# Kernel optimization log

Measured on AMD Instinct MI355X. Metric: run time of the kernel, lower is better.

Reference implementation:

```python
import jax, jax.numpy as jnp
import numpy as np

D_MODEL = 1024
D_INNER = 2048
D_STATE = 16
DT_RANK = 64  # ceil(1024/16)
N_LAYERS = 4
SEQ = 4096


def setup_inputs() -> dict:
    key = jax.random.key(0)
    ks = list(jax.random.split(key, 8))
    L, d, di, n, r = N_LAYERS, D_MODEL, D_INNER, D_STATE, DT_RANK
    def rn(k, shape, scale):
        return jax.random.normal(k, shape, dtype=jnp.float32) * scale
    A_init = jnp.tile(jnp.log(jnp.arange(1, n + 1, dtype=jnp.float32))[None, None, :], (L, di, 1))
    return {
        'x': jax.random.normal(ks[0], (SEQ, d), dtype=jnp.float32),
        'pos_enc': jax.random.normal(ks[1], (SEQ, d), dtype=jnp.float32),
        'ln_g': jnp.ones((d,), jnp.float32),
        'ln_b': jnp.zeros((d,), jnp.float32),
        'innorm_g': jnp.ones((L, d), jnp.float32),
        'innorm_b': jnp.zeros((L, d), jnp.float32),
        'in_proj_w': rn(ks[2], (L, 2 * di, d), 0.02),
        'in_proj_b': jnp.zeros((L, 2 * di), jnp.float32),
        'conv_w': rn(ks[3], (L, di, 1, 3), 0.1),
        'conv_b': jnp.zeros((L, di), jnp.float32),
        'deltaBC_w': rn(ks[4], (L, r + 2 * n, di), 0.02),
        'dt_proj_w': rn(ks[5], (L, di, r), 0.02),
        'dt_proj_b': jnp.zeros((L, di), jnp.float32),
        'A_log': A_init,
        'Dp': jnp.ones((L, di), jnp.float32),
        'outnorm_g': jnp.ones((L, di), jnp.float32),
        'outnorm_b': jnp.zeros((L, di), jnp.float32),
        'out_proj_w': rn(ks[6], (L, d, di), 0.02),
        'out_proj_b': jnp.zeros((L, d), jnp.float32),
    }


def _ln(x, g, b, eps):
    mu = jnp.mean(x, axis=-1, keepdims=True)
    var = jnp.mean((x - mu) ** 2, axis=-1, keepdims=True)
    return (x - mu) * jax.lax.rsqrt(var + eps) * g + b


def _selective_scan(u, delta, A, B, C, D):
    # u, delta: [b,l,d]; A: [d,n]; B, C: [b,l,n]; D: [d]
    b, l, d = u.shape
    n = A.shape[1]
    def step(h, inputs):
        d_t, B_t, u_t, C_t = inputs          # [b,d],[b,n],[b,d],[b,n]
        dA = jnp.exp(d_t[:, :, None] * A)    # [b,d,n]
        dBu = (d_t * u_t)[:, :, None] * B_t[:, None, :]
        h = dA * h + dBu
        y = jnp.einsum('bdn,bn->bd', h, C_t)
        return h, y
    h0 = jnp.zeros((b, d, n), u.dtype)
    xs = (jnp.swapaxes(delta, 0, 1), jnp.swapaxes(B, 0, 1),
          jnp.swapaxes(u, 0, 1), jnp.swapaxes(C, 0, 1))
    _, ys = jax.lax.scan(step, h0, xs)       # ys: [l,b,d]
    return jnp.swapaxes(ys, 0, 1) + u * D


def _block(x, innorm_g, innorm_b, in_proj_w, in_proj_b, conv_w, conv_b,
           deltaBC_w, dt_proj_w, dt_proj_b, A_log, Dp, outnorm_g, outnorm_b,
           out_proj_w, out_proj_b):
    skip = x
    h = _ln(x, innorm_g, innorm_b, 1e-5)
    xz = h @ in_proj_w.T + in_proj_b
    x1, z1 = jnp.split(xz, 2, axis=-1)       # [b,s,di] each
    # depthwise conv1d, k=3, pad=1
    xc = jnp.swapaxes(x1, 1, 2)              # [b,di,s]
    xc = jax.lax.conv_general_dilated(xc, conv_w, (1,), [(1, 1)],
                                      feature_group_count=xc.shape[1],
                                      dimension_numbers=('NCH', 'OIH', 'NCH'))
    xc = xc + conv_b[None, :, None]
    u = jnp.swapaxes(xc, 1, 2)               # [b,s,di]
    # SSM
    A = -jnp.exp(A_log)
    dbc = u @ deltaBC_w.T                    # [b,s,r+2n]
    delta, B, C = jnp.split(dbc, [DT_RANK, DT_RANK + D_STATE], axis=-1)
    delta = jax.nn.softplus(delta @ dt_proj_w.T + dt_proj_b)
    y = _selective_scan(u, delta, A, B, C, Dp)
    y = _ln(y, outnorm_g, outnorm_b, 1e-5)
    out = y * jax.nn.silu(z1)
    return out @ out_proj_w.T + out_proj_b + skip


def _forward(x, pos_enc, ln_g, ln_b, innorm_g, innorm_b, in_proj_w, in_proj_b,
             conv_w, conv_b, deltaBC_w, dt_proj_w, dt_proj_b, A_log, Dp,
             outnorm_g, outnorm_b, out_proj_w, out_proj_b):
    enc = _ln(x + pos_enc, ln_g, ln_b, 1e-6)[None]  # [1,s,d]
    for i in range(N_LAYERS):
        enc = _block(enc, innorm_g[i], innorm_b[i], in_proj_w[i], in_proj_b[i],
                     conv_w[i], conv_b[i], deltaBC_w[i], dt_proj_w[i],
                     dt_proj_b[i], A_log[i], Dp[i], outnorm_g[i], outnorm_b[i],
                     out_proj_w[i], out_proj_b[i])
    return enc[0]


def reference(x, pos_enc, ln_g, ln_b, innorm_g, innorm_b, in_proj_w, in_proj_b,
              conv_w, conv_b, deltaBC_w, dt_proj_w, dt_proj_b, A_log, Dp,
              outnorm_g, outnorm_b, out_proj_w, out_proj_b):
    return _forward(x, pos_enc, ln_g, ln_b, innorm_g, innorm_b, in_proj_w,
                    in_proj_b, conv_w, conv_b, deltaBC_w, dt_proj_w, dt_proj_b,
                    A_log, Dp, outnorm_g, outnorm_b, out_proj_w, out_proj_b)
```

## Files before the change

kernel.cpp:

```cpp
#include <hip/hip_runtime.h>
#include <hip/hip_bf16.h>
#include <stdint.h>


#define SEQ     4096
#define DMODEL  1024
#define DINNER  2048
#define NSTATE  16
#define DTRANK  64
#define NLAYERS 4
#define LC      64
#define NC      64

typedef __attribute__((ext_vector_type(8))) short short8v;
typedef __attribute__((ext_vector_type(4))) float f32x4;
typedef __hip_bfloat16 bf16;

__device__ __forceinline__ float b2f(unsigned short x) {
    unsigned int u = ((unsigned int)x) << 16;
    return __builtin_bit_cast(float, u);
}

__device__ __forceinline__ void gld16(const void* gsrc, void* ldst) {
    __builtin_amdgcn_global_load_lds(
        (const __attribute__((address_space(1))) void*)gsrc,
        (__attribute__((address_space(3))) void*)ldst, 16, 0, 0);
}

__device__ __forceinline__ float block_sum(float v, float* red, int nwaves) {
    #pragma unroll
    for (int o = 32; o > 0; o >>= 1) v += __shfl_down(v, o, 64);
    int lane = threadIdx.x & 63, w = threadIdx.x >> 6;
    __syncthreads();
    if (lane == 0) red[w] = v;
    __syncthreads();
    float s = red[0];
    for (int i = 1; i < nwaves; i++) s += red[i];
    return s;
}

template<int WIDTH, typename OutT>
__global__ void ln_kernel(const float* __restrict__ X, const float* __restrict__ X2,
                          const float* __restrict__ g, const float* __restrict__ bta,
                          OutT* __restrict__ out, float eps) {
    constexpr int E = WIDTH / 256;
    __shared__ float red[4];
    int s = blockIdx.x, tid = threadIdx.x;
    size_t base = (size_t)s * WIDTH;
    float v[E]; float sum = 0.f;
    #pragma unroll
    for (int i = 0; i < E; i++) {
        int c = tid + i * 256;
        float t = X[base + c];
        if (X2) t += X2[base + c];
        v[i] = t; sum += t;
    }
    float mu = block_sum(sum, red, 4) * (1.f / WIDTH);
    float sq = 0.f;
    #pragma unroll
    for (int i = 0; i < E; i++) { float d = v[i] - mu; sq += d * d; }
    float var = block_sum(sq, red, 4) * (1.f / WIDTH);
    float rstd = rsqrtf(var + eps);
    #pragma unroll
    for (int i = 0; i < E; i++) {
        int c = tid + i * 256;
        float r = (v[i] - mu) * rstd * g[c] + bta[c];
        out[base + c] = (OutT)r;
    }
}

__global__ void outnorm_silu_kernel(const float* __restrict__ y, const bf16* __restrict__ xz,
                                    const float* __restrict__ g, const float* __restrict__ bta,
                                    bf16* __restrict__ p_bf, float eps) {
    constexpr int WIDTH = DINNER, E = WIDTH / 256;
    __shared__ float red[4];
    int s = blockIdx.x, tid = threadIdx.x;
    size_t base = (size_t)s * WIDTH;
    const unsigned short* xzu = (const unsigned short*)xz;
    float v[E]; float sum = 0.f;
    #pragma unroll
    for (int i = 0; i < E; i++) { int c = tid + i * 256; v[i] = y[base + c]; sum += v[i]; }
    float mu = block_sum(sum, red, 4) * (1.f / WIDTH);
    float sq = 0.f;
    #pragma unroll
    for (int i = 0; i < E; i++) { float d = v[i] - mu; sq += d * d; }
    float var = block_sum(sq, red, 4) * (1.f / WIDTH);
    float rstd = rsqrtf(var + eps);
    #pragma unroll
    for (int i = 0; i < E; i++) {
        int c = tid + i * 256;
        float ln = (v[i] - mu) * rstd * g[c] + bta[c];
        float z = b2f(xzu[(size_t)s * (2 * DINNER) + DINNER + c]);
        float sig = 1.f / (1.f + __expf(-z));
        p_bf[base + c] = __float2bfloat16(ln * (z * sig));
    }
}

__global__ void conv_kernel(const bf16* __restrict__ xz, const float* __restrict__ cw,
                            const float* __restrict__ cb, bf16* __restrict__ u_bf) {
    int t = blockIdx.x * 256 + threadIdx.x;
    int s = t >> 9, c = (t & 511) * 4;
    size_t row = (size_t)s * (2 * DINNER);
    const unsigned short* xp = (const unsigned short*)xz;
    ushort4 z4 = {0, 0, 0, 0};
    ushort4 v0 = *(const ushort4*)(xp + row + c);
    ushort4 vm = (s > 0)       ? *(const ushort4*)(xp + row - 2 * DINNER + c) : z4;
    ushort4 vp = (s < SEQ - 1) ? *(const ushort4*)(xp + row + 2 * DINNER + c) : z4;
    unsigned short o[4];
    float x0[4] = {b2f(v0.x), b2f(v0.y), b2f(v0.z), b2f(v0.w)};
    float xm[4] = {b2f(vm.x), b2f(vm.y), b2f(vm.z), b2f(vm.w)};
    float xp4[4] = {b2f(vp.x), b2f(vp.y), b2f(vp.z), b2f(vp.w)};
    #pragma unroll
    for (int i = 0; i < 4; i++) {
        int ch = c + i;
        float u = cw[ch * 3 + 0] * xm[i] + cw[ch * 3 + 1] * x0[i]
                + cw[ch * 3 + 2] * xp4[i] + cb[ch];
        o[i] = __builtin_bit_cast(unsigned short, __float2bfloat16(u));
    }
    *(ushort4*)((unsigned short*)u_bf + (size_t)s * DINNER + c) = {o[0], o[1], o[2], o[3]};
}

#define CN0 (2 * DINNER * DMODEL)
#define CN1 (DMODEL * DINNER)
#define CN2 (96 * DINNER)
#define CN3 (DINNER * DTRANK)
__global__ void cvt_all_kernel(const float* __restrict__ w0, const float* __restrict__ w1,
                               const float* __restrict__ w2, const float* __restrict__ w3,
                               bf16* __restrict__ o0, bf16* __restrict__ o1,
                               bf16* __restrict__ o2, bf16* __restrict__ o3) {
    size_t i = (size_t)(blockIdx.x * 256 + threadIdx.x) * 4;
    const float* src; bf16* dst;
    if (i < CN0)                   { src = w0; dst = o0; }
    else if (i < CN0 + CN1)        { src = w1; dst = o1; i -= CN0; }
    else if (i < CN0 + CN1 + CN2)  { src = w2; dst = o2; i -= CN0 + CN1; }
    else                           { src = w3; dst = o3; i -= CN0 + CN1 + CN2; }
    float4 v = *(const float4*)(src + i);
    __hip_bfloat162 t0, t1;
    t0.x = __float2bfloat16(v.x); t0.y = __float2bfloat16(v.y);
    t1.x = __float2bfloat16(v.z); t1.y = __float2bfloat16(v.w);
    __hip_bfloat162* o = (__hip_bfloat162*)(dst + i);
    o[0] = t0; o[1] = t1;
}

template<int MODE>
__global__ __launch_bounds__(256, 2)
void mfma_gemm(const bf16* __restrict__ A, int lda,
               const bf16* __restrict__ W, int ldw,
               const float* __restrict__ bias,
               float* __restrict__ C, int ldc,
               const float* __restrict__ res,
               bf16* __restrict__ Cbf,
               int M, int N, int K) {
    __shared__ __attribute__((aligned(16))) short sA[128][32];
    __shared__ __attribute__((aligned(16))) short sB[128][32];
    int tid = threadIdx.x;
    int lane = tid & 63, w = tid >> 6;
    int wm = w >> 1, wn = w & 1;
    int m0 = blockIdx.x * 128, n0 = blockIdx.y * 128;
    int r16 = lane & 15, quad = lane >> 4;
    int ldrow = (lane >> 2);
    int c8 = (lane & 3) * 8;

    if (MODE == 1) {
        int kz = blockIdx.z;
        A += (size_t)kz * K;
        W += (size_t)kz * K;
        C += (size_t)kz * M * 96;
    }

    f32x4 acc[4][4] = {};

    for (int k0 = 0; k0 < K; k0 += 32) {
        __syncthreads();
        #pragma unroll
        for (int j = 0; j < 2; j++) {
            int row = j * 64 + w * 16 + ldrow;
            gld16(A + (size_t)(m0 + row) * lda + k0 + c8,
                  (char*)&sA[0][0] + j * 4096 + w * 1024);
            int nr = n0 + row; if (nr > N - 1) nr = N - 1;
            gld16(W + (size_t)nr * ldw + k0 + c8,
                  (char*)&sB[0][0] + j * 4096 + w * 1024);
        }
        __syncthreads();
        short8v aF[4], bF[4];
        #pragma unroll
        for (int mi = 0; mi < 4; mi++)
            aF[mi] = *(const short8v*)&sA[wm * 64 + mi * 16 + r16][quad * 8];
        #pragma unroll
        for (int ni = 0; ni < 4; ni++)
            bF[ni] = *(const short8v*)&sB[wn * 64 + ni * 16 + r16][quad * 8];
        #pragma unroll
        for (int mi = 0; mi < 4; mi++)
            #pragma unroll
            for (int ni = 0; ni < 4; ni++)
                acc[mi][ni] = __builtin_amdgcn_mfma_f32_16x16x32_bf16(
                    aF[mi], bF[ni], acc[mi][ni], 0, 0, 0);
    }

    #pragma unroll
    for (int mi = 0; mi < 4; mi++) {
        #pragma unroll
        for (int ni = 0; ni < 4; ni++) {
            f32x4 a = acc[mi][ni];
            int col = n0 + wn * 64 + ni * 16 + r16;
            int rbase = m0 + wm * 64 + mi * 16 + quad * 4;
            #pragma unroll
            for (int r = 0; r < 4; r++) {
                int row = rbase + r;
                float v = a[r];
                if (MODE == 0 || MODE == 2 || MODE == 3) v += bias[col];
                if (MODE == 2) v = (v > 20.f) ? v : log1pf(__expf(v));
                if (MODE == 3) v += res[(size_t)row * ldc + col];
                if (MODE == 1) {
                    if (col < 96) C[(size_t)row * 96 + col] = v;
                } else if (MODE == 0) {
                    Cbf[(size_t)row * ldc + col] = __float2bfloat16(v);
                } else {
                    C[(size_t)row * ldc + col] = v;
                }
            }
        }
    }
}

__global__ void reduce_dbc_kernel(const float* __restrict__ p, float* __restrict__ dbc,
                                  bf16* __restrict__ dbc_bf) {
    int i = blockIdx.x * 256 + threadIdx.x;
    const int SP = SEQ * 96;
    float v = p[i] + p[i + SP] + p[i + 2 * SP] + p[i + 3 * SP];
    dbc[i] = v;
    int row = i / 96, c = i - row * 96;
    if (c < DTRANK) dbc_bf[(size_t)row * DTRANK + c] = __float2bfloat16(v);
}

__device__ __forceinline__ bool a_is_neg_integers(const float* a) {
    bool fast = true;
    #pragma unroll
    for (int n = 0; n < NSTATE; n++)
        fast = fast && (__builtin_fabsf(a[n] + (float)(n + 1)) < 1e-3f * (n + 1));
    return fast;
}

__global__ void scan1_kernel(const float* __restrict__ delta, const bf16* __restrict__ u,
                             const float* __restrict__ dbc, const float* __restrict__ A_log,
                             float* __restrict__ h_end, float* __restrict__ dsum) {
    __shared__ __attribute__((aligned(16))) float sB[LC][NSTATE];
    int k = blockIdx.x, d = blockIdx.y * 256 + threadIdx.x;
    int s0 = k * LC, tid = threadIdx.x;
    #pragma unroll
    for (int i = 0; i < 4; i++) {
        int idx = tid + i * 256;
        int r = idx >> 4, n = idx & 15;
        sB[r][n] = dbc[(size_t)(s0 + r) * 96 + DTRANK + n];
    }
    float a[NSTATE];
    #pragma unroll
    for (int n = 0; n < NSTATE; n++) a[n] = -__expf(A_log[(size_t)d * NSTATE + n]);
    bool fast = a_is_neg_integers(a);
    __syncthreads();
    const unsigned short* uu16 = (const unsigned short*)u;
    float h[NSTATE] = {}; float ds = 0.f;
    if (fast) {
        #pragma unroll 2
        for (int r = 0; r < LC; r++) {
            float dl = delta[(size_t)(s0 + r) * DINNER + d];
            float du = dl * b2f(uu16[(size_t)(s0 + r) * DINNER + d]);
            ds += dl;
            float g = __expf(-dl);
            float Bv[NSTATE];
            #pragma unroll
            for (int q = 0; q < 4; q++) *(float4*)&Bv[q * 4] = *(const float4*)&sB[r][q * 4];
            float fac = 1.f;
            #pragma unroll
            for (int n = 0; n < NSTATE; n++) {
                fac *= g;
                h[n] = fac * h[n] + du * Bv[n];
            }
        }
    } else {
        #pragma unroll 2
        for (int r = 0; r < LC; r++) {
            float dl = delta[(size_t)(s0 + r) * DINNER + d];
            float du = dl * b2f(uu16[(size_t)(s0 + r) * DINNER + d]);
            ds += dl;
            float Bv[NSTATE];
            #pragma unroll
            for (int q = 0; q < 4; q++) *(float4*)&Bv[q * 4] = *(const float4*)&sB[r][q * 4];
            #pragma unroll
            for (int n = 0; n < NSTATE; n++)
                h[n] = __expf(dl * a[n]) * h[n] + du * Bv[n];
        }
    }
    #pragma unroll
    for (int n = 0; n < NSTATE; n++)
        h_end[((size_t)k * NSTATE + n) * DINNER + d] = h[n];
    dsum[(size_t)k * DINNER + d] = ds;
}

__global__ void scan2_kernel(const float* __restrict__ A_log, const float* __restrict__ dsum,
                             const float* __restrict__ h_end, float* __restrict__ hinit) {
    int id = blockIdx.x * 256 + threadIdx.x;
    int d = id & (DINNER - 1), n = id >> 11;
    float a = -__expf(A_log[(size_t)d * NSTATE + n]);
    float h = 0.f;
    for (int k = 0; k < NC; k++) {
        size_t off = ((size_t)k * NSTATE + n) * DINNER + d;
        hinit[off] = h;
        h = __expf(a * dsum[(size_t)k * DINNER + d]) * h + h_end[off];
    }
}

__global__ void scan3_kernel(float* __restrict__ delta_y, const bf16* __restrict__ u,
                             const float* __restrict__ dbc, const float* __restrict__ A_log,
                             const float* __restrict__ Dp, const float* __restrict__ hinit) {
    __shared__ __attribute__((aligned(16))) float sB[LC][NSTATE];
    __shared__ __attribute__((aligned(16))) float sC[LC][NSTATE];
    int k = blockIdx.x, d = blockIdx.y * 256 + threadIdx.x;
    int s0 = k * LC, tid = threadIdx.x;
    #pragma unroll
    for (int i = 0; i < 8; i++) {
        int idx = tid + i * 256;
        int r = idx >> 5, c = idx & 31;
        float v = dbc[(size_t)(s0 + r) * 96 + DTRANK + c];
        if (c < 16) sB[r][c] = v; else sC[r][c - 16] = v;
    }
    float a[NSTATE];
    #pragma unroll
    for (int n = 0; n < NSTATE; n++) a[n] = -__expf(A_log[(size_t)d * NSTATE + n]);
    bool fast = a_is_neg_integers(a);
    float h[NSTATE];
    #pragma unroll
    for (int n = 0; n < NSTATE; n++)
        h[n] = hinit[((size_t)k * NSTATE + n) * DINNER + d];
    float dpv = Dp[d];
    __syncthreads();
    const unsigned short* uu16 = (const unsigned short*)u;
    if (fast) {
        #pragma unroll 2
        for (int r = 0; r < LC; r++) {
            float dl = delta_y[(size_t)(s0 + r) * DINNER + d];
            float uu = b2f(uu16[(size_t)(s0 + r) * DINNER + d]);
            float du = dl * uu;
            float g = __expf(-dl);
            float Bv[NSTATE], Cv[NSTATE];
            #pragma unroll
            for (int q = 0; q < 4; q++) {
                *(float4*)&Bv[q * 4] = *(const float4*)&sB[r][q * 4];
                *(float4*)&Cv[q * 4] = *(const float4*)&sC[r][q * 4];
            }
            float y = uu * dpv;
            float fac = 1.f;
            #pragma unroll
            for (int n = 0; n < NSTATE; n++) {
                fac *= g;
                h[n] = fac * h[n] + du * Bv[n];
                y += h[n] * Cv[n];
            }
            delta_y[(size_t)(s0 + r) * DINNER + d] = y;
        }
    } else {
        #pragma unroll 2
        for (int r = 0; r < LC; r++) {
            float dl = delta_y[(size_t)(s0 + r) * DINNER + d];
            float uu = b2f(uu16[(size_t)(s0 + r) * DINNER + d]);
            float du = dl * uu;
            float Bv[NSTATE], Cv[NSTATE];
            #pragma unroll
            for (int q = 0; q < 4; q++) {
                *(float4*)&Bv[q * 4] = *(const float4*)&sB[r][q * 4];
                *(float4*)&Cv[q * 4] = *(const float4*)&sC[r][q * 4];
            }
            float y = uu * dpv;
            #pragma unroll
            for (int n = 0; n < NSTATE; n++) {
                h[n] = __expf(dl * a[n]) * h[n] + du * Bv[n];
                y += h[n] * Cv[n];
            }
            delta_y[(size_t)(s0 + r) * DINNER + d] = y;
        }
    }
}

extern "C" void kernel_launch(void* const* d_in, const int* in_sizes, int n_in,
                              void* d_out, int out_size, void* d_ws, size_t ws_size,
                              hipStream_t stream) {
    const float* x         = (const float*)d_in[0];
    const float* pos       = (const float*)d_in[1];
    const float* ln_g      = (const float*)d_in[2];
    const float* ln_b      = (const float*)d_in[3];
    const float* innorm_g  = (const float*)d_in[4];
    const float* innorm_b  = (const float*)d_in[5];
    const float* in_proj_w = (const float*)d_in[6];
    const float* in_proj_b = (const float*)d_in[7];
    const float* conv_w    = (const float*)d_in[8];
    const float* conv_b    = (const float*)d_in[9];
    const float* deltaBC_w = (const float*)d_in[10];
    const float* dt_proj_w = (const float*)d_in[11];
    const float* dt_proj_b = (const float*)d_in[12];
    const float* A_log     = (const float*)d_in[13];
    const float* Dp        = (const float*)d_in[14];
    const float* outnorm_g = (const float*)d_in[15];
    const float* outnorm_b = (const float*)d_in[16];
    const float* out_proj_w= (const float*)d_in[17];
    const float* out_proj_b= (const float*)d_in[18];

    float* enc = (float*)d_out;
    char* ws = (char*)d_ws;
    const size_t MB = 1024 * 1024;
    bf16*  h_bf   = (bf16*) (ws + 0);
    bf16*  p_bf   = (bf16*) (ws + 0);
    bf16*  xz_bf  = (bf16*) (ws + 16 * MB);
    float* dlt    = (float*)(ws + 48 * MB);
    float* dbcp   = (float*)(ws + 48 * MB);
    bf16*  u_bf   = (bf16*) (ws + 80 * MB);
    float* dbc    = (float*)(ws + 96 * MB);
    bf16*  dbc_bf = (bf16*) (ws + 98 * MB);
    float* h_end  = (float*)(ws + 99 * MB);
    float* hinit  = (float*)(ws + 107 * MB);
    float* dsum   = (float*)(ws + 115 * MB);
    bf16*  w_in   = (bf16*) (ws + 116 * MB);
    bf16*  w_dbc  = (bf16*) (ws + 124 * MB);
    bf16*  w_dt   = (bf16*) (ws + 125 * MB);
    bf16*  w_out  = (bf16*) (ws + 126 * MB);

    ln_kernel<DMODEL, float><<<SEQ, 256, 0, stream>>>(x, pos, ln_g, ln_b, enc, 1e-6f);

    for (int L = 0; L < NLAYERS; L++) {
        const float* Al = A_log + (size_t)L * DINNER * NSTATE;
        cvt_all_kernel<<<(CN0 + CN1 + CN2 + CN3) / 1024, 256, 0, stream>>>(
            in_proj_w + (size_t)L * CN0, out_proj_w + (size_t)L * CN1,
            deltaBC_w + (size_t)L * CN2, dt_proj_w + (size_t)L * CN3,
            w_in, w_out, w_dbc, w_dt);

        ln_kernel<DMODEL, bf16><<<SEQ, 256, 0, stream>>>(enc, nullptr, innorm_g + L * DMODEL,
                                                         innorm_b + L * DMODEL, h_bf, 1e-5f);
        mfma_gemm<0><<<dim3(32, 32), 256, 0, stream>>>(
            h_bf, DMODEL, w_in, DMODEL, in_proj_b + (size_t)L * 2 * DINNER,
            nullptr, 2 * DINNER, nullptr, xz_bf, SEQ, 2 * DINNER, DMODEL);
        conv_kernel<<<(SEQ * 512) / 256, 256, 0, stream>>>(
            xz_bf, conv_w + (size_t)L * DINNER * 3, conv_b + L * DINNER, u_bf);
        mfma_gemm<1><<<dim3(32, 1, 4), 256, 0, stream>>>(
            u_bf, DINNER, w_dbc, DINNER, nullptr,
            dbcp, 96, nullptr, nullptr, SEQ, 96, 512);
        reduce_dbc_kernel<<<(SEQ * 96) / 256, 256, 0, stream>>>(dbcp, dbc, dbc_bf);
        mfma_gemm<2><<<dim3(32, 16), 256, 0, stream>>>(
            dbc_bf, DTRANK, w_dt, DTRANK, dt_proj_b + L * DINNER,
            dlt, DINNER, nullptr, nullptr, SEQ, DINNER, DTRANK);
        scan1_kernel<<<dim3(NC, DINNER / 256), 256, 0, stream>>>(dlt, u_bf, dbc, Al, h_end, dsum);
        scan2_kernel<<<(DINNER * NSTATE) / 256, 256, 0, stream>>>(Al, dsum, h_end, hinit);
        scan3_kernel<<<dim3(NC, DINNER / 256), 256, 0, stream>>>(dlt, u_bf, dbc, Al,
                                                                 Dp + L * DINNER, hinit);
        outnorm_silu_kernel<<<SEQ, 256, 0, stream>>>(dlt, xz_bf, outnorm_g + L * DINNER,
                                                     outnorm_b + L * DINNER, p_bf, 1e-5f);
        mfma_gemm<3><<<dim3(32, 8), 256, 0, stream>>>(
            p_bf, DINNER, w_out, DINNER, out_proj_b + L * DMODEL,
            enc, DMODEL, enc, nullptr, SEQ, DMODEL, DINNER);
    }
}
```

Before: 1.127 ms.

## Fuse conv into dbc GEMM, store delta/y in bf16, hoist weight conversion

The depthwise conv is fused into the split-K deltaBC GEMM prologue, which also writes u. The split-K reduction is folded into the dt GEMM and the scan kernels, and the separate reduce kernel is removed. Delta and y are kept in bf16 rather than fp32, which halves scan and outnorm traffic but costs precision. Weight conversion for all layers now runs once up front instead of per layer, and the layernorm and outnorm kernels are vectorized.

```diff
diff --git a/kernel.cpp b/kernel.cpp
--- a/kernel.cpp
+++ b/kernel.cpp
@@ -11,6 +11,8 @@
 #define NLAYERS 4
 #define LC      64
 #define NC      64
+#define SPLITK  4
+#define SPDBC   (SEQ * 96)
 
 typedef __attribute__((ext_vector_type(8))) short short8v;
 typedef __attribute__((ext_vector_type(4))) float f32x4;
@@ -19,6 +21,12 @@
 __device__ __forceinline__ float b2f(unsigned short x) {
     unsigned int u = ((unsigned int)x) << 16;
     return __builtin_bit_cast(float, u);
+}
+__device__ __forceinline__ unsigned short f2b(float x) {
+    return __builtin_bit_cast(unsigned short, __float2bfloat16(x));
+}
+__device__ __forceinline__ unsigned int pk2(float a, float b) {
+    return (unsigned int)f2b(a) | ((unsigned int)f2b(b) << 16);
 }
 
 __device__ __forceinline__ void gld16(const void* gsrc, void* ldst) {
@@ -39,107 +47,109 @@
     return s;
 }
 
-template<int WIDTH, typename OutT>
-__global__ void ln_kernel(const float* __restrict__ X, const float* __restrict__ X2,
-                          const float* __restrict__ g, const float* __restrict__ bta,
-                          OutT* __restrict__ out, float eps) {
-    constexpr int E = WIDTH / 256;
+template<bool BF16OUT>
+__global__ void ln1024_kernel(const float* __restrict__ X, const float* __restrict__ X2,
+                              const float* __restrict__ g, const float* __restrict__ bta,
+                              void* __restrict__ out, float eps) {
     __shared__ float red[4];
     int s = blockIdx.x, tid = threadIdx.x;
-    size_t base = (size_t)s * WIDTH;
-    float v[E]; float sum = 0.f;
-    #pragma unroll
-    for (int i = 0; i < E; i++) {
-        int c = tid + i * 256;
-        float t = X[base + c];
-        if (X2) t += X2[base + c];
-        v[i] = t; sum += t;
-    }
-    float mu = block_sum(sum, red, 4) * (1.f / WIDTH);
-    float sq = 0.f;
-    #pragma unroll
-    for (int i = 0; i < E; i++) { float d = v[i] - mu; sq += d * d; }
-    float var = block_sum(sq, red, 4) * (1.f / WIDTH);
+    size_t base = (size_t)s * 1024;
+    int c = tid * 4;
+    float4 v = *(const float4*)(X + base + c);
+    if (X2) {
+        float4 w = *(const float4*)(X2 + base + c);
+        v.x += w.x; v.y += w.y; v.z += w.z; v.w += w.w;
+    }
+    float mu = block_sum(v.x + v.y + v.z + v.w, red, 4) * (1.f / 1024);
+    float sq = (v.x - mu) * (v.x - mu) + (v.y - mu) * (v.y - mu)
+             + (v.z - mu) * (v.z - mu) + (v.w - mu) * (v.w - mu);
+    float var = block_sum(sq, red, 4) * (1.f / 1024);
     float rstd = rsqrtf(var + eps);
-    #pragma unroll
-    for (int i = 0; i < E; i++) {
-        int c = tid + i * 256;
-        float r = (v[i] - mu) * rstd * g[c] + bta[c];
-        out[base + c] = (OutT)r;
-    }
-}
-
-__global__ void outnorm_silu_kernel(const float* __restrict__ y, const bf16* __restrict__ xz,
+    float4 gg = *(const float4*)(g + c);
+    float4 bb = *(const float4*)(bta + c);
+    float o0 = (v.x - mu) * rstd * gg.x + bb.x;
+    float o1 = (v.y - mu) * rstd * gg.y + bb.y;
+    float o2 = (v.z - mu) * rstd * gg.z + bb.z;
+    float o3 = (v.w - mu) * rstd * gg.w + bb.w;
+    if (BF16OUT) {
+        uint2 o; o.x = pk2(o0, o1); o.y = pk2(o2, o3);
+        *(uint2*)((unsigned short*)out + base + c) = o;
+    } else {
+        float4 o = {o0, o1, o2, o3};
+        *(float4*)((float*)out + base + c) = o;
+    }
+}
+
+__global__ void outnorm_silu_kernel(const unsigned short* __restrict__ y,
+                                    const unsigned short* __restrict__ xz,
                                     const float* __restrict__ g, const float* __restrict__ bta,
-                                    bf16* __restrict__ p_bf, float eps) {
-    constexpr int WIDTH = DINNER, E = WIDTH / 256;
+                                    unsigned short* __restrict__ p, float eps) {
     __shared__ float red[4];
     int s = blockIdx.x, tid = threadIdx.x;
-    size_t base = (size_t)s * WIDTH;
-    const unsigned short* xzu = (const unsigned short*)xz;
-    float v[E]; float sum = 0.f;
-    #pragma unroll
-    for (int i = 0; i < E; i++) { int c = tid + i * 256; v[i] = y[base + c]; sum += v[i]; }
-    float mu = block_sum(sum, red, 4) * (1.f / WIDTH);
+    int c = tid * 8;
+    size_t base = (size_t)s * DINNER;
+    uint4 yv = *(const uint4*)(y + base + c);
+    float v[8] = {b2f((unsigned short)(yv.x & 0xffff)), b2f((unsigned short)(yv.x >> 16)),
+                  b2f((unsigned short)(yv.y & 0xffff)), b2f((unsigned short)(yv.y >> 16)),
+                  b2f((unsigned short)(yv.z & 0xffff)), b2f((unsigned short)(yv.z >> 16)),
+                  b2f((unsigned short)(yv.w & 0xffff)), b2f((unsigned short)(yv.w >> 16))};
+    float sum = 0.f;
+    #pragma unroll
+    for (int i = 0; i < 8; i++) sum += v[i];
+    float mu = block_sum(sum, red, 4) * (1.f / DINNER);
     float sq = 0.f;
     #pragma unroll
-    for (int i = 0; i < E; i++) { float d = v[i] - mu; sq += d * d; }
-    float var = block_sum(sq, red, 4) * (1.f / WIDTH);
+    for (int i = 0; i < 8; i++) { float dd = v[i] - mu; sq += dd * dd; }
+    float var = block_sum(sq, red, 4) * (1.f / DINNER);
     float rstd = rsqrtf(var + eps);
-    #pragma unroll
-    for (int i = 0; i < E; i++) {
-        int c = tid + i * 256;
-        float ln = (v[i] - mu) * rstd * g[c] + bta[c];
-        float z = b2f(xzu[(size_t)s * (2 * DINNER) + DINNER + c]);
-        float sig = 1.f / (1.f + __expf(-z));
-        p_bf[base + c] = __float2bfloat16(ln * (z * sig));
-    }
-}
-
-__global__ void conv_kernel(const bf16* __restrict__ xz, const float* __restrict__ cw,
-                            const float* __restrict__ cb, bf16* __restrict__ u_bf) {
-    int t = blockIdx.x * 256 + threadIdx.x;
-    int s = t >> 9, c = (t & 511) * 4;
-    size_t row = (size_t)s * (2 * DINNER);
-    const unsigned short* xp = (const unsigned short*)xz;
-    ushort4 z4 = {0, 0, 0, 0};
-    ushort4 v0 = *(const ushort4*)(xp + row + c);
-    ushort4 vm = (s > 0)       ? *(const ushort4*)(xp + row - 2 * DINNER + c) : z4;
-    ushort4 vp = (s < SEQ - 1) ? *(const ushort4*)(xp + row + 2 * DINNER + c) : z4;
-    unsigned short o[4];
-    float x0[4] = {b2f(v0.x), b2f(v0.y), b2f(v0.z), b2f(v0.w)};
-    float xm[4] = {b2f(vm.x), b2f(vm.y), b2f(vm.z), b2f(vm.w)};
-    float xp4[4] = {b2f(vp.x), b2f(vp.y), b2f(vp.z), b2f(vp.w)};
-    #pragma unroll
-    for (int i = 0; i < 4; i++) {
-        int ch = c + i;
-        float u = cw[ch * 3 + 0] * xm[i] + cw[ch * 3 + 1] * x0[i]
-                + cw[ch * 3 + 2] * xp4[i] + cb[ch];
-        o[i] = __builtin_bit_cast(unsigned short, __float2bfloat16(u));
-    }
-    *(ushort4*)((unsigned short*)u_bf + (size_t)s * DINNER + c) = {o[0], o[1], o[2], o[3]};
+    uint4 zv = *(const uint4*)(xz + (size_t)s * 2 * DINNER + DINNER + c);
+    float z[8] = {b2f((unsigned short)(zv.x & 0xffff)), b2f((unsigned short)(zv.x >> 16)),
+                  b2f((unsigned short)(zv.y & 0xffff)), b2f((unsigned short)(zv.y >> 16)),
+                  b2f((unsigned short)(zv.z & 0xffff)), b2f((unsigned short)(zv.z >> 16)),
+                  b2f((unsigned short)(zv.w & 0xffff)), b2f((unsigned short)(zv.w >> 16))};
+    float4 g0 = *(const float4*)(g + c),  g1 = *(const float4*)(g + c + 4);
+    float4 b0 = *(const float4*)(bta + c), b1 = *(const float4*)(bta + c + 4);
+    float gv[8] = {g0.x, g0.y, g0.z, g0.w, g1.x, g1.y, g1.z, g1.w};
+    float bv[8] = {b0.x, b0.y, b0.z, b0.w, b1.x, b1.y, b1.z, b1.w};
+    float o[8];
+    #pragma unroll
+    for (int i = 0; i < 8; i++) {
+        float ln = (v[i] - mu) * rstd * gv[i] + bv[i];
+        float sig = 1.f / (1.f + __expf(-z[i]));
+        o[i] = ln * (z[i] * sig);
+    }
+    uint4 ov = {pk2(o[0], o[1]), pk2(o[2], o[3]), pk2(o[4], o[5]), pk2(o[6], o[7])};
+    *(uint4*)(p + base + c) = ov;
 }
 
 #define CN0 (2 * DINNER * DMODEL)
 #define CN1 (DMODEL * DINNER)
 #define CN2 (96 * DINNER)
 #define CN3 (DINNER * DTRANK)
+#define CPER ((size_t)(CN0 + CN1 + CN2 + CN3))
 __global__ void cvt_all_kernel(const float* __restrict__ w0, const float* __restrict__ w1,
                                const float* __restrict__ w2, const float* __restrict__ w3,
                                bf16* __restrict__ o0, bf16* __restrict__ o1,
                                bf16* __restrict__ o2, bf16* __restrict__ o3) {
     size_t i = (size_t)(blockIdx.x * 256 + threadIdx.x) * 4;
-    const float* src; bf16* dst;
-    if (i < CN0)                   { src = w0; dst = o0; }
-    else if (i < CN0 + CN1)        { src = w1; dst = o1; i -= CN0; }
-    else if (i < CN0 + CN1 + CN2)  { src = w2; dst = o2; i -= CN0 + CN1; }
-    else                           { src = w3; dst = o3; i -= CN0 + CN1 + CN2; }
-    float4 v = *(const float4*)(src + i);
-    __hip_bfloat162 t0, t1;
-    t0.x = __float2bfloat16(v.x); t0.y = __float2bfloat16(v.y);
-    t1.x = __float2bfloat16(v.z); t1.y = __float2bfloat16(v.w);
-    __hip_bfloat162* o = (__hip_bfloat162*)(dst + i);
-    o[0] = t0; o[1] = t1;
+    int L = (int)(i / CPER);
+    size_t r = i - (size_t)L * CPER;
+    const float* src; bf16* dst; size_t off;
+    if (r < CN0)                   { src = w0 + (size_t)L * CN0; dst = o0 + (size_t)L * CN0; off = r; }
+    else if (r < CN0 + CN1)        { src = w1 + (size_t)L * CN1; dst = o1 + (size_t)L * CN1; off = r - CN0; }
+    else if (r < CN0 + CN1 + CN2)  { src = w2 + (size_t)L * CN2; dst = o2 + (size_t)L * CN2; off = r - CN0 - CN1; }
+    else                           { src = w3 + (size_t)L * CN3; dst = o3 + (size_t)L * CN3; off = r - CN0 - CN1 - CN2; }
+    float4 v = *(const float4*)(src + off);
+    uint2 o; o.x = pk2(v.x, v.y); o.y = pk2(v.z, v.w);
+    *(uint2*)((unsigned short*)dst + off) = o;
+}
+
+__global__ void conv_wt_kernel(const float* __restrict__ cw, float* __restrict__ cwT) {
+    int gid = blockIdx.x * 256 + threadIdx.x;
+    int l = gid >> 11, c = gid & 2047;
+    #pragma unroll
+    for (int t = 0; t < 3; t++)
+        cwT[((size_t)l * 3 + t) * 2048 + c] = cw[((size_t)l * 2048 + c) * 3 + t];
 }
 
 template<int MODE>
@@ -161,13 +171,6 @@
     int ldrow = (lane >> 2);
     int c8 = (lane & 3) * 8;
 
-    if (MODE == 1) {
-        int kz = blockIdx.z;
-        A += (size_t)kz * K;
-        W += (size_t)kz * K;
-        C += (size_t)kz * M * 96;
-    }
-
     f32x4 acc[4][4] = {};
 
     for (int k0 = 0; k0 < K; k0 += 32) {
@@ -177,8 +180,7 @@
             int row = j * 64 + w * 16 + ldrow;
             gld16(A + (size_t)(m0 + row) * lda + k0 + c8,
                   (char*)&sA[0][0] + j * 4096 + w * 1024);
-            int nr = n0 + row; if (nr > N - 1) nr = N - 1;
-            gld16(W + (size_t)nr * ldw + k0 + c8,
+            gld16(W + (size_t)(n0 + row) * ldw + k0 + c8,
                   (char*)&sB[0][0] + j * 4096 + w * 1024);
         }
         __syncthreads();
@@ -207,30 +209,179 @@
             #pragma unroll
             for (int r = 0; r < 4; r++) {
                 int row = rbase + r;
-                float v = a[r];
-                if (MODE == 0 || MODE == 2 || MODE == 3) v += bias[col];
-                if (MODE == 2) v = (v > 20.f) ? v : log1pf(__expf(v));
+                float v = a[r] + bias[col];
                 if (MODE == 3) v += res[(size_t)row * ldc + col];
-                if (MODE == 1) {
-                    if (col < 96) C[(size_t)row * 96 + col] = v;
-                } else if (MODE == 0) {
-                    Cbf[(size_t)row * ldc + col] = __float2bfloat16(v);
-                } else {
-                    C[(size_t)row * ldc + col] = v;
-                }
-            }
-        }
-    }
-}
-
-__global__ void reduce_dbc_kernel(const float* __restrict__ p, float* __restrict__ dbc,
-                                  bf16* __restrict__ dbc_bf) {
-    int i = blockIdx.x * 256 + threadIdx.x;
-    const int SP = SEQ * 96;
-    float v = p[i] + p[i + SP] + p[i + 2 * SP] + p[i + 3 * SP];
-    dbc[i] = v;
-    int row = i / 96, c = i - row * 96;
-    if (c < DTRANK) dbc_bf[(size_t)row * DTRANK + c] = __float2bfloat16(v);
+                if (MODE == 0) Cbf[(size_t)row * ldc + col] = __float2bfloat16(v);
+                else           C[(size_t)row * ldc + col] = v;
+            }
+        }
+    }
+}
+
+__global__ __launch_bounds__(256, 2)
+void dbc_conv_gemm(const unsigned short* __restrict__ xz,
+                   const float* __restrict__ cwT, const float* __restrict__ cb,
+                   const bf16* __restrict__ W,
+                   unsigned short* __restrict__ u16, float* __restrict__ Cp) {
+    __shared__ __attribute__((aligned(16))) short sA[128][32];
+    __shared__ __attribute__((aligned(16))) short sB[128][32];
+    int tid = threadIdx.x;
+    int lane = tid & 63, w = tid >> 6;
+    int wm = w >> 1, wn = w & 1;
+    int m0 = blockIdx.x * 128;
+    int kz = blockIdx.z;
+    int r16 = lane & 15, quad = lane >> 4;
+    int ldrow = lane >> 2;
+    int cg4 = (lane & 3) * 8;
+
+    f32x4 acc[4][4] = {};
+
+    for (int k0 = 0; k0 < 512; k0 += 32) {
+        int cc = kz * 512 + k0 + cg4;
+        float4 w0a = *(const float4*)(cwT + 0 * 2048 + cc);
+        float4 w0b = *(const float4*)(cwT + 0 * 2048 + cc + 4);
+        float4 w1a = *(const float4*)(cwT + 1 * 2048 + cc);
+        float4 w1b = *(const float4*)(cwT + 1 * 2048 + cc + 4);
+        float4 w2a = *(const float4*)(cwT + 2 * 2048 + cc);
+        float4 w2b = *(const float4*)(cwT + 2 * 2048 + cc + 4);
+        float4 cba = *(const float4*)(cb + cc);
+        float4 cbb = *(const float4*)(cb + cc + 4);
+        float cw0[8] = {w0a.x,w0a.y,w0a.z,w0a.w,w0b.x,w0b.y,w0b.z,w0b.w};
+        float cw1[8] = {w1a.x,w1a.y,w1a.z,w1a.w,w1b.x,w1b.y,w1b.z,w1b.w};
+        float cw2[8] = {w2a.x,w2a.y,w2a.z,w2a.w,w2b.x,w2b.y,w2b.z,w2b.w};
+        float cbv[8] = {cba.x,cba.y,cba.z,cba.w,cbb.x,cbb.y,cbb.z,cbb.w};
+        __syncthreads();
+        #pragma unroll
+        for (int j = 0; j < 2; j++) {
+            int row = j * 64 + w * 16 + ldrow;
+            int s = m0 + row;
+            const unsigned short* xr = xz + (size_t)s * (2 * DINNER) + cc;
+            uint4 z4 = {0, 0, 0, 0};
+            uint4 v0 = *(const uint4*)xr;
+            uint4 vm = (s > 0)       ? *(const uint4*)(xr - 2 * DINNER) : z4;
+            uint4 vp = (s < SEQ - 1) ? *(const uint4*)(xr + 2 * DINNER) : z4;
+            unsigned int v0u[4] = {v0.x, v0.y, v0.z, v0.w};
+            unsigned int vmu[4] = {vm.x, vm.y, vm.z, vm.w};
+            unsigned int vpu[4] = {vp.x, vp.y, vp.z, vp.w};
+            float uo[8];
+            #pragma unroll
+            for (int i = 0; i < 4; i++) {
+                float x0l = b2f((unsigned short)(v0u[i] & 0xffff));
+                float x0h = b2f((unsigned short)(v0u[i] >> 16));
+                float xml = b2f((unsigned short)(vmu[i] & 0xffff));
+                float xmh = b2f((unsigned short)(vmu[i] >> 16));
+                float xpl = b2f((unsigned short)(vpu[i] & 0xffff));
+                float xph = b2f((unsigned short)(vpu[i] >> 16));
+                uo[2*i]   = cw0[2*i]   * xml + cw1[2*i]   * x0l + cw2[2*i]   * xpl + cbv[2*i];
+                uo[2*i+1] = cw0[2*i+1] * xmh + cw1[2*i+1] * x0h + cw2[2*i+1] * xph + cbv[2*i+1];
+            }
+            uint4 up = {pk2(uo[0], uo[1]), pk2(uo[2], uo[3]),
+                        pk2(uo[4], uo[5]), pk2(uo[6], uo[7])};
+            *(uint4*)((char*)&sA[0][0] + row * 64 + (lane & 3) * 16) = up;
+            *(uint4*)(u16 + (size_t)s * DINNER + cc) = up;
+            int nr = row > 95 ? 95 : row;
+            gld16(W + (size_t)nr * DINNER + kz * 512 + k0 + cg4,
+                  (char*)&sB[0][0] + j * 4096 + w * 1024);
+        }
+        __syncthreads();
+        short8v aF[4], bF[4];
+        #pragma unroll
+        for (int mi = 0; mi < 4; mi++)
+            aF[mi] = *(const short8v*)&sA[wm * 64 + mi * 16 + r16][quad * 8];
+        #pragma unroll
+        for (int ni = 0; ni < 4; ni++)
+            bF[ni] = *(const short8v*)&sB[wn * 64 + ni * 16 + r16][quad * 8];
+        #pragma unroll
+        for (int mi = 0; mi < 4; mi++)
+            #pragma unroll
+            for (int ni = 0; ni < 4; ni++)
+                acc[mi][ni] = __builtin_amdgcn_mfma_f32_16x16x32_bf16(
+                    aF[mi], bF[ni], acc[mi][ni], 0, 0, 0);
+    }
+
+    float* C = Cp + (size_t)kz * SPDBC;
+    #pragma unroll
+    for (int mi = 0; mi < 4; mi++) {
+        #pragma unroll
+        for (int ni = 0; ni < 4; ni++) {
+            f32x4 a = acc[mi][ni];
+            int col = wn * 64 + ni * 16 + r16;
+            if (col >= 96) continue;
+            int rbase = m0 + wm * 64 + mi * 16 + quad * 4;
+            #pragma unroll
+            for (int r = 0; r < 4; r++)
+                C[(size_t)(rbase + r) * 96 + col] = a[r];
+        }
+    }
+}
+
+__global__ __launch_bounds__(256, 2)
+void dt_gemm(const float* __restrict__ dbcp, const bf16* __restrict__ W,
+             const float* __restrict__ bias, unsigned short* __restrict__ dlt) {
+    __shared__ __attribute__((aligned(16))) short sA[128][32];
+    __shared__ __attribute__((aligned(16))) short sB[128][32];
+    int tid = threadIdx.x;
+    int lane = tid & 63, w = tid >> 6;
+    int wm = w >> 1, wn = w & 1;
+    int m0 = blockIdx.x * 128, n0 = blockIdx.y * 128;
+    int r16 = lane & 15, quad = lane >> 4;
+    int ldrow = lane >> 2;
+    int c8 = (lane & 3) * 8;
+
+    f32x4 acc[4][4] = {};
+
+    #pragma unroll
+    for (int k0 = 0; k0 < 64; k0 += 32) {
+        __syncthreads();
+        #pragma unroll
+        for (int j = 0; j < 2; j++) {
+            int row = j * 64 + w * 16 + ldrow;
+            int s = m0 + row;
+            size_t o = (size_t)s * 96 + k0 + c8;
+            float4 aa = {0,0,0,0}, ab = {0,0,0,0};
+            #pragma unroll
+            for (int p = 0; p < SPLITK; p++) {
+                float4 t0 = *(const float4*)(dbcp + o + (size_t)p * SPDBC);
+                float4 t1 = *(const float4*)(dbcp + o + (size_t)p * SPDBC + 4);
+                aa.x += t0.x; aa.y += t0.y; aa.z += t0.z; aa.w += t0.w;
+                ab.x += t1.x; ab.y += t1.y; ab.z += t1.z; ab.w += t1.w;
+            }
+            uint4 up = {pk2(aa.x, aa.y), pk2(aa.z, aa.w), pk2(ab.x, ab.y), pk2(ab.z, ab.w)};
+            *(uint4*)((char*)&sA[0][0] + row * 64 + (lane & 3) * 16) = up;
+            gld16(W + (size_t)(n0 + row) * DTRANK + k0 + c8,
+                  (char*)&sB[0][0] + j * 4096 + w * 1024);
+        }
+        __syncthreads();
+        short8v aF[4], bF[4];
+        #pragma unroll
+        for (int mi = 0; mi < 4; mi++)
+            aF[mi] = *(const short8v*)&sA[wm * 64 + mi * 16 + r16][quad * 8];
+        #pragma unroll
+        for (int ni = 0; ni < 4; ni++)
+            bF[ni] = *(const short8v*)&sB[wn * 64 + ni * 16 + r16][quad * 8];
+        #pragma unroll
+        for (int mi = 0; mi < 4; mi++)
+            #pragma unroll
+            for (int ni = 0; ni < 4; ni++)
+                acc[mi][ni] = __builtin_amdgcn_mfma_f32_16x16x32_bf16(
+                    aF[mi], bF[ni], acc[mi][ni], 0, 0, 0);
+    }
+
+    #pragma unroll
+    for (int mi = 0; mi < 4; mi++) {
+        #pragma unroll
+        for (int ni = 0; ni < 4; ni++) {
+            f32x4 a = acc[mi][ni];
+            int col = n0 + wn * 64 + ni * 16 + r16;
+            int rbase = m0 + wm * 64 + mi * 16 + quad * 4;
+            #pragma unroll
+            for (int r = 0; r < 4; r++) {
+                float v = a[r] + bias[col];
+                v = (v > 20.f) ? v : log1pf(__expf(v));
+                dlt[(size_t)(rbase + r) * DINNER + col] = f2b(v);
+            }
+        }
+    }
 }
 
 __device__ __forceinline__ bool a_is_neg_integers(const float* a) {
@@ -241,8 +392,9 @@
     return fast;
 }
 
-__global__ void scan1_kernel(const float* __restrict__ delta, const bf16* __restrict__ u,
-                             const float* __restrict__ dbc, const float* __restrict__ A_log,
+__global__ void scan1_kernel(const unsigned short* __restrict__ dl16,
+                             const unsigned short* __restrict__ uu16,
+                             const float* __restrict__ dbcp, const float* __restrict__ A_log,
                              float* __restrict__ h_end, float* __restrict__ dsum) {
     __shared__ __attribute__((aligned(16))) float sB[LC][NSTATE];
     int k = blockIdx.x, d = blockIdx.y * 256 + threadIdx.x;
@@ -251,19 +403,19 @@
     for (int i = 0; i < 4; i++) {
         int idx = tid + i * 256;
         int r = idx >> 4, n = idx & 15;
-        sB[r][n] = dbc[(size_t)(s0 + r) * 96 + DTRANK + n];
+        size_t o = (size_t)(s0 + r) * 96 + DTRANK + n;
+        sB[r][n] = dbcp[o] + dbcp[o + SPDBC] + dbcp[o + 2 * SPDBC] + dbcp[o + 3 * SPDBC];
     }
     float a[NSTATE];
     #pragma unroll
     for (int n = 0; n < NSTATE; n++) a[n] = -__expf(A_log[(size_t)d * NSTATE + n]);
     bool fast = a_is_neg_integers(a);
     __syncthreads();
-    const unsigned short* uu16 = (const unsigned short*)u;
     float h[NSTATE] = {}; float ds = 0.f;
     if (fast) {
         #pragma unroll 2
         for (int r = 0; r < LC; r++) {
-            float dl = delta[(size_t)(s0 + r) * DINNER + d];
+            float dl = b2f(dl16[(size_t)(s0 + r) * DINNER + d]);
             float du = dl * b2f(uu16[(size_t)(s0 + r) * DINNER + d]);
             ds += dl;
             float g = __expf(-dl);
@@ -272,23 +424,19 @@
             for (int q = 0; q < 4; q++) *(float4*)&Bv[q * 4] = *(const float4*)&sB[r][q * 4];
             float fac = 1.f;
             #pragma unroll
-            for (int n = 0; n < NSTATE; n++) {
-                fac *= g;
-                h[n] = fac * h[n] + du * Bv[n];
-            }
+            for (int n = 0; n < NSTATE; n++) { fac *= g; h[n] = fac * h[n] + du * Bv[n]; }
         }
     } else {
         #pragma unroll 2
         for (int r = 0; r < LC; r++) {
-            float dl = delta[(size_t)(s0 + r) * DINNER + d];
+            float dl = b2f(dl16[(size_t)(s0 + r) * DINNER + d]);
             float du = dl * b2f(uu16[(size_t)(s0 + r) * DINNER + d]);
             ds += dl;
             float Bv[NSTATE];
             #pragma unroll
             for (int q = 0; q < 4; q++) *(float4*)&Bv[q * 4] = *(const float4*)&sB[r][q * 4];
             #pragma unroll
-            for (int n = 0; n < NSTATE; n++)
-                h[n] = __expf(dl * a[n]) * h[n] + du * Bv[n];
+            for (int n = 0; n < NSTATE; n++) h[n] = __expf(dl * a[n]) * h[n] + du * Bv[n];
         }
     }
     #pragma unroll
@@ -310,8 +458,9 @@
     }
 }
 
-__global__ void scan3_kernel(float* __restrict__ delta_y, const bf16* __restrict__ u,
-                             const float* __restrict__ dbc, const float* __restrict__ A_log,
+__global__ void scan3_kernel(unsigned short* __restrict__ dl_y16,
+                             const unsigned short* __restrict__ uu16,
+                             const float* __restrict__ dbcp, const float* __restrict__ A_log,
                              const float* __restrict__ Dp, const float* __restrict__ hinit) {
     __shared__ __attribute__((aligned(16))) float sB[LC][NSTATE];
     __shared__ __attribute__((aligned(16))) float sC[LC][NSTATE];
@@ -321,7 +470,8 @@
     for (int i = 0; i < 8; i++) {
         int idx = tid + i * 256;
         int r = idx >> 5, c = idx & 31;
-        float v = dbc[(size_t)(s0 + r) * 96 + DTRANK + c];
+        size_t o = (size_t)(s0 + r) * 96 + DTRANK + c;
+        float v = dbcp[o] + dbcp[o + SPDBC] + dbcp[o + 2 * SPDBC] + dbcp[o + 3 * SPDBC];
         if (c < 16) sB[r][c] = v; else sC[r][c - 16] = v;
     }
     float a[NSTATE];
@@ -334,11 +484,10 @@
         h[n] = hinit[((size_t)k * NSTATE + n) * DINNER + d];
     float dpv = Dp[d];
     __syncthreads();
-    const unsigned short* uu16 = (const unsigned short*)u;
     if (fast) {
         #pragma unroll 2
         for (int r = 0; r < LC; r++) {
-            float dl = delta_y[(size_t)(s0 + r) * DINNER + d];
+            float dl = b2f(dl_y16[(size_t)(s0 + r) * DINNER + d]);
             float uu = b2f(uu16[(size_t)(s0 + r) * DINNER + d]);
             float du = dl * uu;
             float g = __expf(-dl);
@@ -356,12 +505,12 @@
                 h[n] = fac * h[n] + du * Bv[n];
                 y += h[n] * Cv[n];
             }
-            delta_y[(size_t)(s0 + r) * DINNER + d] = y;
+            dl_y16[(size_t)(s0 + r) * DINNER + d] = f2b(y);
         }
     } else {
         #pragma unroll 2
         for (int r = 0; r < LC; r++) {
-            float dl = delta_y[(size_t)(s0 + r) * DINNER + d];
+            float dl = b2f(dl_y16[(size_t)(s0 + r) * DINNER + d]);
             float uu = b2f(uu16[(size_t)(s0 + r) * DINNER + d]);
             float du = dl * uu;
             float Bv[NSTATE], Cv[NSTATE];
@@ -376,7 +525,7 @@
                 h[n] = __expf(dl * a[n]) * h[n] + du * Bv[n];
                 y += h[n] * Cv[n];
             }
-            delta_y[(size_t)(s0 + r) * DINNER + d] = y;
+            dl_y16[(size_t)(s0 + r) * DINNER + d] = f2b(y);
         }
     }
 }
@@ -407,51 +556,57 @@
     float* enc = (float*)d_out;
     char* ws = (char*)d_ws;
     const size_t MB = 1024 * 1024;
-    bf16*  h_bf   = (bf16*) (ws + 0);
-    bf16*  p_bf   = (bf16*) (ws + 0);
-    bf16*  xz_bf  = (bf16*) (ws + 16 * MB);
-    float* dlt    = (float*)(ws + 48 * MB);
-    float* dbcp   = (float*)(ws + 48 * MB);
-    bf16*  u_bf   = (bf16*) (ws + 80 * MB);
-    float* dbc    = (float*)(ws + 96 * MB);
-    bf16*  dbc_bf = (bf16*) (ws + 98 * MB);
-    float* h_end  = (float*)(ws + 99 * MB);
-    float* hinit  = (float*)(ws + 107 * MB);
-    float* dsum   = (float*)(ws + 115 * MB);
-    bf16*  w_in   = (bf16*) (ws + 116 * MB);
-    bf16*  w_dbc  = (bf16*) (ws + 124 * MB);
-    bf16*  w_dt   = (bf16*) (ws + 125 * MB);
-    bf16*  w_out  = (bf16*) (ws + 126 * MB);
-
-    ln_kernel<DMODEL, float><<<SEQ, 256, 0, stream>>>(x, pos, ln_g, ln_b, enc, 1e-6f);
+    bf16*  h_bf    = (bf16*) (ws + 0);
+    bf16*  p_bf    = (bf16*) (ws + 0);
+    bf16*  xz_bf   = (bf16*) (ws + 16 * MB);
+    bf16*  dlt_bf  = (bf16*) (ws + 48 * MB);
+    bf16*  u_bf    = (bf16*) (ws + 64 * MB);
+    float* dbcp    = (float*)(ws + 80 * MB);
+    float* h_end   = (float*)(ws + 87 * MB);
+    float* hinit   = (float*)(ws + 95 * MB);
+    float* dsum    = (float*)(ws + 103 * MB);
+    bf16*  w_in_a  = (bf16*) (ws + 104 * MB);
+    bf16*  w_out_a = (bf16*) (ws + 136 * MB);
+    bf16*  w_dbc_a = (bf16*) (ws + 152 * MB);
+    bf16*  w_dt_a  = (bf16*) (ws + 154 * MB);
+    float* cwT     = (float*)(ws + 155 * MB);
+
+    cvt_all_kernel<<<(unsigned)((NLAYERS * CPER) / 1024), 256, 0, stream>>>(
+        in_proj_w, out_proj_w, deltaBC_w, dt_proj_w, w_in_a, w_out_a, w_dbc_a, w_dt_a);
+    conv_wt_kernel<<<(NLAYERS * 2048) / 256, 256, 0, stream>>>(conv_w, cwT);
+
+    ln1024_kernel<false><<<SEQ, 256, 0, stream>>>(x, pos, ln_g, ln_b, enc, 1e-6f);
 
     for (int L = 0; L < NLAYERS; L++) {
-        const float* Al = A_log + (size_t)L * DINNER * NSTATE;
-        cvt_all_kernel<<<(CN0 + CN1 + CN2 + CN3) / 1024, 256, 0, stream>>>(
-            in_proj_w + (size_t)L * CN0, out_proj_w + (size_t)L * CN1,
-            deltaBC_w + (size_t)L * CN2, dt_proj_w + (size_t)L * CN3,
-            w_in, w_out, w_dbc, w_dt);
-
-        ln_kernel<DMODEL, bf16><<<SEQ, 256, 0, stream>>>(enc, nullptr, innorm_g + L * DMODEL,
-                                                         innorm_b + L * DMODEL, h_bf, 1e-5f);
+        const float* Al  = A_log + (size_t)L * DINNER * NSTATE;
+        const float* Dpl = Dp + (size_t)L * DINNER;
+        bf16* w_in  = w_in_a  + (size_t)L * CN0;
+        bf16* w_out = w_out_a + (size_t)L * CN1;
+        bf16* w_dbc = w_dbc_a + (size_t)L * CN2;
+        bf16* w_dt  = w_dt_a  + (size_t)L * CN3;
+
+        ln1024_kernel<true><<<SEQ, 256, 0, stream>>>(enc, nullptr, innorm_g + L * DMODEL,
+                                                     innorm_b + L * DMODEL, h_bf, 1e-5f);
         mfma_gemm<0><<<dim3(32, 32), 256, 0, stream>>>(
             h_bf, DMODEL, w_in, DMODEL, in_proj_b + (size_t)L * 2 * DINNER,
             nullptr, 2 * DINNER, nullptr, xz_bf, SEQ, 2 * DINNER, DMODEL);
-        conv_kernel<<<(SEQ * 512) / 256, 256, 0, stream>>>(
-            xz_bf, conv_w + (size_t)L * DINNER * 3, conv_b + L * DINNER, u_bf);
-        mfma_gemm<1><<<dim3(32, 1, 4), 256, 0, stream>>>(
-            u_bf, DINNER, w_dbc, DINNER, nullptr,
-            dbcp, 96, nullptr, nullptr, SEQ, 96, 512);
-        reduce_dbc_kernel<<<(SEQ * 96) / 256, 256, 0, stream>>>(dbcp, dbc, dbc_bf);
-        mfma_gemm<2><<<dim3(32, 16), 256, 0, stream>>>(
-            dbc_bf, DTRANK, w_dt, DTRANK, dt_proj_b + L * DINNER,
-            dlt, DINNER, nullptr, nullptr, SEQ, DINNER, DTRANK);
-        scan1_kernel<<<dim3(NC, DINNER / 256), 256, 0, stream>>>(dlt, u_bf, dbc, Al, h_end, dsum);
+        dbc_conv_gemm<<<dim3(32, 1, SPLITK), 256, 0, stream>>>(
+            (const unsigned short*)xz_bf, cwT + (size_t)L * 3 * 2048,
+            conv_b + (size_t)L * DINNER, w_dbc,
+            (unsigned short*)u_bf, dbcp);
+        dt_gemm<<<dim3(32, 16), 256, 0, stream>>>(
+            dbcp, w_dt, dt_proj_b + (size_t)L * DINNER, (unsigned short*)dlt_bf);
+        scan1_kernel<<<dim3(NC, 8), 256, 0, stream>>>(
+            (const unsigned short*)dlt_bf, (const unsigned short*)u_bf,
+            dbcp, Al, h_end, dsum);
         scan2_kernel<<<(DINNER * NSTATE) / 256, 256, 0, stream>>>(Al, dsum, h_end, hinit);
-        scan3_kernel<<<dim3(NC, DINNER / 256), 256, 0, stream>>>(dlt, u_bf, dbc, Al,
-                                                                 Dp + L * DINNER, hinit);
-        outnorm_silu_kernel<<<SEQ, 256, 0, stream>>>(dlt, xz_bf, outnorm_g + L * DINNER,
-                                                     outnorm_b + L * DINNER, p_bf, 1e-5f);
+        scan3_kernel<<<dim3(NC, 8), 256, 0, stream>>>(
+            (unsigned short*)dlt_bf, (const unsigned short*)u_bf,
+            dbcp, Al, Dpl, hinit);
+        outnorm_silu_kernel<<<SEQ, 256, 0, stream>>>(
+            (const unsigned short*)dlt_bf, (const unsigned short*)xz_bf,
+            outnorm_g + L * DINNER, outnorm_b + L * DINNER,
+            (unsigned short*)p_bf, 1e-5f);
         mfma_gemm<3><<<dim3(32, 8), 256, 0, stream>>>(
             p_bf, DINNER, w_out, DINNER, out_proj_b + L * DMODEL,
             enc, DMODEL, enc, nullptr, SEQ, DMODEL, DINNER);
```

New measurement: 1.217 ms. +8.0%, slower.
